# Kernel tuning notes

Hardware: AMD Instinct MI355X
Metric: run time of the kernel (lower is better)

## Reference

```python
import jax, jax.numpy as jnp
import numpy as np

B, IN_DIM, LATENT = 1024, 256, 256


def _linear_params(key, fan_in, fan_out):
    # torch nn.Linear default init: U(-1/sqrt(fan_in), 1/sqrt(fan_in))
    k1, k2 = jax.random.split(key)
    lim = 1.0 / np.sqrt(fan_in)
    W = jax.random.uniform(k1, (fan_out, fan_in), minval=-lim, maxval=lim, dtype=jnp.float32)
    b = jax.random.uniform(k2, (fan_out,), minval=-lim, maxval=lim, dtype=jnp.float32)
    return W, b


def setup_inputs() -> dict:
    key = jax.random.key(0)
    ks = jax.random.split(key, 8)
    Wd1, bd1 = _linear_params(ks[0], IN_DIM, LATENT)
    Wd2, bd2 = _linear_params(ks[1], LATENT, LATENT)
    Wu1, bu1 = _linear_params(ks[2], IN_DIM, LATENT)
    Wu2, bu2 = _linear_params(ks[3], LATENT, LATENT)
    Wm1, bm1 = _linear_params(ks[4], IN_DIM, LATENT)
    Wm2, bm2 = _linear_params(ks[5], LATENT, LATENT)
    x = jax.random.normal(ks[6], (B, IN_DIM), dtype=jnp.float32)
    v = jax.random.normal(ks[7], (B, LATENT), dtype=jnp.float32)  # noise from calculate_z
    return {
        "x": x,
        "Wd1": Wd1, "bd1": bd1, "Wd2": Wd2, "bd2": bd2,
        "Wu1": Wu1, "bu1": bu1, "Wu2": Wu2, "bu2": bu2,
        "Wm1": Wm1, "bm1": bm1, "Wm2": Wm2, "bm2": bm2,
        "v": v,
    }


def reference(x, Wd1, bd1, Wd2, bd2, Wu1, bu1, Wu2, bu2, Wm1, bm1, Wm2, bm2, v):
    sig = jax.nn.sigmoid
    # three small 2-layer MLPs
    d = sig(sig(x @ Wd1.T + bd1) @ Wd2.T + bd2)          # [B, n]
    u = sig(sig(x @ Wu1.T + bu1) @ Wu2.T + bu2)          # [B, n]
    mean = jnp.tanh(jnp.tanh(x @ Wm1.T + bm1) @ Wm2.T + bm2)  # [B, n]

    # calculate_r: inverse of diag_embed(d) is diag(1/d); +epsilon is added to ALL
    # entries (as in the original torch code), making D_inv a full matrix.
    EPS = 1e-6
    n = d.shape[-1]
    eye = jnp.eye(n, dtype=d.dtype)
    D_inv = (1.0 / d)[..., None] * eye + EPS               # [B, n, n]
    D_in_sqr = jnp.sqrt(D_inv)                             # elementwise sqrt
    U = u[:, :, None] * u[:, None, :]                      # rank-1 [B, n, n]
    ut_d_inv_u = jnp.einsum('bi,bij,bj->b', u, D_inv, u)[:, None, None]  # [B,1,1]
    eta = 1.0 / (1.0 + ut_d_inv_u)
    right = (1.0 - jnp.sqrt(eta)) / ut_d_inv_u
    R = D_in_sqr - right * jnp.matmul(D_inv, jnp.matmul(U, D_in_sqr))  # [B, n, n]

    # calculate_z
    z = jnp.einsum('bij,bj->bi', R, v) + mean              # [B, n]
    return (mean, R, z)
```

## Files before the change

kernel.cpp:

```cpp
#include <hip/hip_runtime.h>
#include <hip/hip_bf16.h>
#include <math.h>

#define NB 1024
#define N 256
#define NBN (NB * N)
#define EPS 1e-6f
#define SQRT_EPS 1e-3f

typedef short bf16x8 __attribute__((ext_vector_type(8)));
typedef float f32x4  __attribute__((ext_vector_type(4)));

__device__ __forceinline__ float fast_rcp(float x) {
    return __builtin_amdgcn_rcpf(x);
}
__device__ __forceinline__ float sigmoidf(float x) {
    return fast_rcp(1.0f + __expf(-x));
}
__device__ __forceinline__ float fast_tanh(float x) {
    float ax = fabsf(x);
    float e  = __expf(2.0f * ax);
    float t  = 1.0f - 2.0f * fast_rcp(e + 1.0f);
    return copysignf(t, x);
}
__device__ __forceinline__ unsigned short to_bf16(float f) {
    __hip_bfloat16 h = __float2bfloat16(f);
    return *(unsigned short*)&h;
}
__device__ __forceinline__ bf16x8 cvt8(float4 f0, float4 f1) {
    bf16x8 a;
    a[0] = (short)to_bf16(f0.x); a[1] = (short)to_bf16(f0.y);
    a[2] = (short)to_bf16(f0.z); a[3] = (short)to_bf16(f0.w);
    a[4] = (short)to_bf16(f1.x); a[5] = (short)to_bf16(f1.y);
    a[6] = (short)to_bf16(f1.z); a[7] = (short)to_bf16(f1.w);
    return a;
}

__global__ __launch_bounds__(768) void l1_kernel(
    const float* __restrict__ x,
    const float* __restrict__ Wd1, const float* __restrict__ Wu1,
    const float* __restrict__ Wm1,
    const float* __restrict__ bd1, const float* __restrict__ bu1,
    const float* __restrict__ bm1, unsigned short* __restrict__ h1g)
{
    const int tid = threadIdx.x;
    const int w   = tid >> 6;
    const int mlp = w >> 2;
    const int sub = w & 3;
    const int l   = tid & 63;
    const int ml  = l & 15;
    const int kg  = l >> 4;
    const int b0  = (blockIdx.x >> 2) * 16;
    const int n0  = (blockIdx.x & 3) * 64 + sub * 16;
    const int n   = n0 + ml;

    bf16x8 af[8];
    {
        const float* xrow = x + (size_t)(b0 + ml) * N;
        #pragma unroll
        for (int kq = 0; kq < 8; ++kq) {
            float4 f0 = *(const float4*)(xrow + kq * 32 + kg * 8);
            float4 f1 = *(const float4*)(xrow + kq * 32 + kg * 8 + 4);
            af[kq] = cvt8(f0, f1);
        }
    }
    const float* Wl = (mlp == 0) ? Wd1 : (mlp == 1) ? Wu1 : Wm1;
    const float* wrow = Wl + (size_t)n * N;
    f32x4 acc = {0.f, 0.f, 0.f, 0.f};
    #pragma unroll
    for (int kq = 0; kq < 8; ++kq) {
        float4 f0 = *(const float4*)(wrow + kq * 32 + kg * 8);
        float4 f1 = *(const float4*)(wrow + kq * 32 + kg * 8 + 4);
        bf16x8 bf = cvt8(f0, f1);
        acc = __builtin_amdgcn_mfma_f32_16x16x32_bf16(af[kq], bf, acc, 0, 0, 0);
    }
    const float* bias = (mlp == 0) ? bd1 : (mlp == 1) ? bu1 : bm1;
    const float bb = bias[n];
    #pragma unroll
    for (int reg = 0; reg < 4; ++reg) {
        const int row = b0 + kg * 4 + reg;
        float val = acc[reg] + bb;
        float act = (mlp < 2) ? sigmoidf(val) : fast_tanh(val);
        h1g[(size_t)mlp * NBN + (size_t)row * N + n] = to_bf16(act);
    }
}

__global__ __launch_bounds__(768) void l2_kernel(
    const unsigned short* __restrict__ h1g,
    const float* __restrict__ Wd2, const float* __restrict__ Wu2,
    const float* __restrict__ Wm2,
    const float* __restrict__ bd2, const float* __restrict__ bu2,
    const float* __restrict__ bm2, float* __restrict__ h2g)
{
    const int tid = threadIdx.x;
    const int w   = tid >> 6;
    const int mlp = w >> 2;
    const int sub = w & 3;
    const int l   = tid & 63;
    const int ml  = l & 15;
    const int kg  = l >> 4;
    const int b0  = (blockIdx.x >> 2) * 16;
    const int n0  = (blockIdx.x & 3) * 64 + sub * 16;
    const int n   = n0 + ml;

    bf16x8 af[8];
    {
        const unsigned short* arow = h1g + (size_t)mlp * NBN + (size_t)(b0 + ml) * N;
        #pragma unroll
        for (int kq = 0; kq < 8; ++kq)
            af[kq] = *(const bf16x8*)(arow + kq * 32 + kg * 8);
    }
    const float* Wl = (mlp == 0) ? Wd2 : (mlp == 1) ? Wu2 : Wm2;
    const float* wrow = Wl + (size_t)n * N;
    f32x4 acc = {0.f, 0.f, 0.f, 0.f};
    #pragma unroll
    for (int kq = 0; kq < 8; ++kq) {
        float4 f0 = *(const float4*)(wrow + kq * 32 + kg * 8);
        float4 f1 = *(const float4*)(wrow + kq * 32 + kg * 8 + 4);
        bf16x8 bf = cvt8(f0, f1);
        acc = __builtin_amdgcn_mfma_f32_16x16x32_bf16(af[kq], bf, acc, 0, 0, 0);
    }
    const float* bias = (mlp == 0) ? bd2 : (mlp == 1) ? bu2 : bm2;
    const float bb = bias[n];
    #pragma unroll
    for (int reg = 0; reg < 4; ++reg) {
        const int row = b0 + kg * 4 + reg;
        float val = acc[reg] + bb;
        float act = (mlp < 2) ? sigmoidf(val) : fast_tanh(val);
        h2g[(size_t)mlp * NBN + (size_t)row * N + n] = act;
    }
}

__global__ __launch_bounds__(256) void r_epi_kernel(
    const float* __restrict__ h2g, const float* __restrict__ v,
    float* __restrict__ out_mean, float* __restrict__ out_z,
    float* __restrict__ R)
{
    __shared__ float s_lds[N];
    __shared__ float a_lds[64];
    __shared__ float tp_lds[64];
    __shared__ float red1[4][3];
    __shared__ float red2[4];

    const int tid   = threadIdx.x;
    const int b     = blockIdx.x >> 2;
    const int chunk = blockIdx.x & 3;
    const int ibase = chunk * 64;
    const int lane  = tid & 63;
    const int wv    = tid >> 6;

    const float d_ = h2g[(size_t)0 * NBN + (size_t)b * N + tid];
    const float u_ = h2g[(size_t)1 * NBN + (size_t)b * N + tid];
    const float m_ = h2g[(size_t)2 * NBN + (size_t)b * N + tid];
    const float vv = v[(size_t)b * N + tid];
    const float inv_d = fast_rcp(d_);

    float s0 = u_, s1 = u_ * u_ * inv_d, s2 = vv;
    #pragma unroll
    for (int off = 32; off > 0; off >>= 1) {
        s0 += __shfl_down(s0, off, 64);
        s1 += __shfl_down(s1, off, 64);
        s2 += __shfl_down(s2, off, 64);
    }
    if (lane == 0) { red1[wv][0] = s0; red1[wv][1] = s1; red1[wv][2] = s2; }
    __syncthreads();
    const float Su = red1[0][0] + red1[1][0] + red1[2][0] + red1[3][0];
    const float qs = red1[0][1] + red1[1][1] + red1[2][1] + red1[3][1];
    const float Sv = red1[0][2] + red1[1][2] + red1[2][2] + red1[3][2];
    const float utDu  = qs + EPS * Su * Su;
    const float sqeta = rsqrtf(1.0f + utDu);
    const float right = (1.0f - sqeta) / utDu;
    const float a  = sqrtf(inv_d + EPS);
    const float s  = u_ * a + SQRT_EPS * (Su - u_);
    const float tp = right * (u_ * inv_d + EPS * Su);

    float sv = s * vv;
    #pragma unroll
    for (int off = 32; off > 0; off >>= 1)
        sv += __shfl_down(sv, off, 64);
    if (lane == 0) red2[wv] = sv;

    s_lds[tid] = s;
    if (tid >= ibase && tid < ibase + 64) {
        a_lds[tid - ibase]  = a;
        tp_lds[tid - ibase] = tp;
    }
    __syncthreads();
    sv = red2[0] + red2[1] + red2[2] + red2[3];

    if (chunk == 0) {
        const size_t idx = (size_t)b * N + tid;
        out_mean[idx] = m_;
        out_z[idx]    = SQRT_EPS * Sv + (a - SQRT_EPS) * vv - tp * sv + m_;
    }

    const int j4 = tid & 63;
    const int il = tid >> 6;
    const float4 svec = ((const float4*)s_lds)[j4];
    float4* Rb = (float4*)(R + (size_t)b * N * N);
    const int jb = j4 * 4;

    #pragma unroll
    for (int it = 0; it < 16; ++it) {
        const int i_loc = it * 4 + il;
        const int i     = ibase + i_loc;
        const float ai  = a_lds[i_loc];
        const float ti  = tp_lds[i_loc];
        float4 o;
        o.x = SQRT_EPS - ti * svec.x;
        o.y = SQRT_EPS - ti * svec.y;
        o.z = SQRT_EPS - ti * svec.z;
        o.w = SQRT_EPS - ti * svec.w;
        if (i >= jb && i < jb + 4) {
            const float add = ai - SQRT_EPS;
            if      (i == jb)     o.x += add;
            else if (i == jb + 1) o.y += add;
            else if (i == jb + 2) o.z += add;
            else                  o.w += add;
        }
        Rb[(size_t)i * 64 + j4] = o;
    }
}

extern "C" void kernel_launch(void* const* d_in, const int* in_sizes, int n_in,
                              void* d_out, int out_size, void* d_ws, size_t ws_size,
                              hipStream_t stream) {
    const float* x   = (const float*)d_in[0];
    const float* Wd1 = (const float*)d_in[1];
    const float* bd1 = (const float*)d_in[2];
    const float* Wd2 = (const float*)d_in[3];
    const float* bd2 = (const float*)d_in[4];
    const float* Wu1 = (const float*)d_in[5];
    const float* bu1 = (const float*)d_in[6];
    const float* Wu2 = (const float*)d_in[7];
    const float* bu2 = (const float*)d_in[8];
    const float* Wm1 = (const float*)d_in[9];
    const float* bm1 = (const float*)d_in[10];
    const float* Wm2 = (const float*)d_in[11];
    const float* bm2 = (const float*)d_in[12];
    const float* v   = (const float*)d_in[13];

    float* out      = (float*)d_out;
    float* out_mean = out;
    float* R        = out + (size_t)NB * N;
    float* out_z    = R + (size_t)NB * N * N;

    unsigned short* h1g = (unsigned short*)d_ws;
    float* h2g = (float*)(h1g + (size_t)3 * NBN);

    l1_kernel<<<256, 768, 0, stream>>>(x, Wd1, Wu1, Wm1, bd1, bu1, bm1, h1g);
    l2_kernel<<<256, 768, 0, stream>>>(h1g, Wd2, Wu2, Wm2, bd2, bu2, bm2, h2g);
    r_epi_kernel<<<NB * 4, 256, 0, stream>>>(h2g, v, out_mean, out_z, R);
}
```

Measured before the change: 72.16 us.

## Merge both MLP layers into one cooperative kernel with grid sync

The two separate layer kernels are combined into a single cooperative launch that uses a grid-wide barrier between layer 1 and layer 2, which removes one kernel launch and its gap. Input rows and layer-1 activations are now staged in shared memory once per block, so each wave reads the shared tile instead of reloading and reconverting global data. The cost is a cooperative-launch requirement and a grid sync. Launch fails if the 256 blocks of 768 threads cannot all be resident at once.

```diff
diff --git a/kernel.cpp b/kernel.cpp
--- a/kernel.cpp
+++ b/kernel.cpp
@@ -1,4 +1,5 @@
 #include <hip/hip_runtime.h>
+#include <hip/hip_cooperative_groups.h>
 #include <hip/hip_bf16.h>
 #include <math.h>
 
@@ -7,6 +8,8 @@
 #define NBN (NB * N)
 #define EPS 1e-6f
 #define SQRT_EPS 1e-3f
+
+namespace cg = cooperative_groups;
 
 typedef short bf16x8 __attribute__((ext_vector_type(8)));
 typedef float f32x4  __attribute__((ext_vector_type(4)));
@@ -36,13 +39,21 @@
     return a;
 }
 
-__global__ __launch_bounds__(768) void l1_kernel(
+__global__ __launch_bounds__(768) void coop_mlp_kernel(
     const float* __restrict__ x,
     const float* __restrict__ Wd1, const float* __restrict__ Wu1,
     const float* __restrict__ Wm1,
+    const float* __restrict__ Wd2, const float* __restrict__ Wu2,
+    const float* __restrict__ Wm2,
     const float* __restrict__ bd1, const float* __restrict__ bu1,
-    const float* __restrict__ bm1, unsigned short* __restrict__ h1g)
+    const float* __restrict__ bm1,
+    const float* __restrict__ bd2, const float* __restrict__ bu2,
+    const float* __restrict__ bm2,
+    unsigned short* __restrict__ h1g, float* __restrict__ h2g)
 {
+    __shared__ unsigned short xa[16][264];
+    __shared__ unsigned short hb[3][16][264];
+
     const int tid = threadIdx.x;
     const int w   = tid >> 6;
     const int mlp = w >> 2;
@@ -50,84 +61,82 @@
     const int l   = tid & 63;
     const int ml  = l & 15;
     const int kg  = l >> 4;
-    const int b0  = (blockIdx.x >> 2) * 16;
-    const int n0  = (blockIdx.x & 3) * 64 + sub * 16;
+    const int b0  = ((int)blockIdx.x >> 2) * 16;
+    const int n0  = ((int)blockIdx.x & 3) * 64 + sub * 16;
     const int n   = n0 + ml;
 
-    bf16x8 af[8];
+    if (tid < 512) {
+        const int row = tid >> 5;
+        const int c8  = tid & 31;
+        const float* src = x + (size_t)(b0 + row) * N + c8 * 8;
+        float4 f0 = *(const float4*)src;
+        float4 f1 = *(const float4*)(src + 4);
+        *(bf16x8*)&xa[row][c8 * 8] = cvt8(f0, f1);
+    }
+    __syncthreads();
+
     {
-        const float* xrow = x + (size_t)(b0 + ml) * N;
+        bf16x8 af[8];
+        #pragma unroll
+        for (int kq = 0; kq < 8; ++kq)
+            af[kq] = *(const bf16x8*)&xa[ml][kq * 32 + kg * 8];
+        const float* Wl = (mlp == 0) ? Wd1 : (mlp == 1) ? Wu1 : Wm1;
+        const float* wrow = Wl + (size_t)n * N;
+        f32x4 acc = {0.f, 0.f, 0.f, 0.f};
         #pragma unroll
         for (int kq = 0; kq < 8; ++kq) {
-            float4 f0 = *(const float4*)(xrow + kq * 32 + kg * 8);
-            float4 f1 = *(const float4*)(xrow + kq * 32 + kg * 8 + 4);
-            af[kq] = cvt8(f0, f1);
-        }
-    }
-    const float* Wl = (mlp == 0) ? Wd1 : (mlp == 1) ? Wu1 : Wm1;
-    const float* wrow = Wl + (size_t)n * N;
-    f32x4 acc = {0.f, 0.f, 0.f, 0.f};
-    #pragma unroll
-    for (int kq = 0; kq < 8; ++kq) {
-        float4 f0 = *(const float4*)(wrow + kq * 32 + kg * 8);
-        float4 f1 = *(const float4*)(wrow + kq * 32 + kg * 8 + 4);
-        bf16x8 bf = cvt8(f0, f1);
-        acc = __builtin_amdgcn_mfma_f32_16x16x32_bf16(af[kq], bf, acc, 0, 0, 0);
-    }
-    const float* bias = (mlp == 0) ? bd1 : (mlp == 1) ? bu1 : bm1;
-    const float bb = bias[n];
-    #pragma unroll
-    for (int reg = 0; reg < 4; ++reg) {
-        const int row = b0 + kg * 4 + reg;
-        float val = acc[reg] + bb;
-        float act = (mlp < 2) ? sigmoidf(val) : fast_tanh(val);
-        h1g[(size_t)mlp * NBN + (size_t)row * N + n] = to_bf16(act);
-    }
-}
-
-__global__ __launch_bounds__(768) void l2_kernel(
-    const unsigned short* __restrict__ h1g,
-    const float* __restrict__ Wd2, const float* __restrict__ Wu2,
-    const float* __restrict__ Wm2,
-    const float* __restrict__ bd2, const float* __restrict__ bu2,
-    const float* __restrict__ bm2, float* __restrict__ h2g)
-{
-    const int tid = threadIdx.x;
-    const int w   = tid >> 6;
-    const int mlp = w >> 2;
-    const int sub = w & 3;
-    const int l   = tid & 63;
-    const int ml  = l & 15;
-    const int kg  = l >> 4;
-    const int b0  = (blockIdx.x >> 2) * 16;
-    const int n0  = (blockIdx.x & 3) * 64 + sub * 16;
-    const int n   = n0 + ml;
-
-    bf16x8 af[8];
+            float4 f0 = *(const float4*)(wrow + kq * 32 + kg * 8);
+            float4 f1 = *(const float4*)(wrow + kq * 32 + kg * 8 + 4);
+            acc = __builtin_amdgcn_mfma_f32_16x16x32_bf16(af[kq], cvt8(f0, f1), acc, 0, 0, 0);
+        }
+        const float* bias = (mlp == 0) ? bd1 : (mlp == 1) ? bu1 : bm1;
+        const float bb = bias[n];
+        #pragma unroll
+        for (int reg = 0; reg < 4; ++reg) {
+            const int row = b0 + kg * 4 + reg;
+            float val = acc[reg] + bb;
+            float act = (mlp < 2) ? sigmoidf(val) : fast_tanh(val);
+            h1g[(size_t)mlp * NBN + (size_t)row * N + n] = to_bf16(act);
+        }
+    }
+
+    cg::this_grid().sync();
+
+    #pragma unroll
+    for (int t = 0; t < 2; ++t) {
+        const int idx = tid * 2 + t;
+        const int m2  = idx >> 9;
+        const int rem = idx & 511;
+        const int row = rem >> 5;
+        const int c8  = rem & 31;
+        *(bf16x8*)&hb[m2][row][c8 * 8] =
+            *(const bf16x8*)(h1g + (size_t)m2 * NBN + (size_t)(b0 + row) * N + c8 * 8);
+    }
+    __syncthreads();
+
     {
-        const unsigned short* arow = h1g + (size_t)mlp * NBN + (size_t)(b0 + ml) * N;
+        bf16x8 af[8];
         #pragma unroll
         for (int kq = 0; kq < 8; ++kq)
-            af[kq] = *(const bf16x8*)(arow + kq * 32 + kg * 8);
-    }
-    const float* Wl = (mlp == 0) ? Wd2 : (mlp == 1) ? Wu2 : Wm2;
-    const float* wrow = Wl + (size_t)n * N;
-    f32x4 acc = {0.f, 0.f, 0.f, 0.f};
-    #pragma unroll
-    for (int kq = 0; kq < 8; ++kq) {
-        float4 f0 = *(const float4*)(wrow + kq * 32 + kg * 8);
-        float4 f1 = *(const float4*)(wrow + kq * 32 + kg * 8 + 4);
-        bf16x8 bf = cvt8(f0, f1);
-        acc = __builtin_amdgcn_mfma_f32_16x16x32_bf16(af[kq], bf, acc, 0, 0, 0);
-    }
-    const float* bias = (mlp == 0) ? bd2 : (mlp == 1) ? bu2 : bm2;
-    const float bb = bias[n];
-    #pragma unroll
-    for (int reg = 0; reg < 4; ++reg) {
-        const int row = b0 + kg * 4 + reg;
-        float val = acc[reg] + bb;
-        float act = (mlp < 2) ? sigmoidf(val) : fast_tanh(val);
-        h2g[(size_t)mlp * NBN + (size_t)row * N + n] = act;
+            af[kq] = *(const bf16x8*)&hb[mlp][ml][kq * 32 + kg * 8];
+        const float* Wl = (mlp == 0) ? Wd2 : (mlp == 1) ? Wu2 : Wm2;
+        const float* wrow = Wl + (size_t)n * N;
+        f32x4 acc = {0.f, 0.f, 0.f, 0.f};
+        #pragma unroll
+        for (int kq = 0; kq < 8; ++kq) {
+            float4 f0 = *(const float4*)(wrow + kq * 32 + kg * 8);
+            float4 f1 = *(const float4*)(wrow + kq * 32 + kg * 8 + 4);
+            acc = __builtin_amdgcn_mfma_f32_16x16x32_bf16(af[kq], cvt8(f0, f1), acc, 0, 0, 0);
+        }
+        const float* bias = (mlp == 0) ? bd2 : (mlp == 1) ? bu2 : bm2;
+        const float bb = bias[n];
+        #pragma unroll
+        for (int reg = 0; reg < 4; ++reg) {
+            const int row = b0 + kg * 4 + reg;
+            float val = acc[reg] + bb;
+            float act = (mlp < 2) ? sigmoidf(val) : fast_tanh(val);
+            h2g[(size_t)mlp * NBN + (size_t)row * N + n] = act;
+        }
     }
 }
 
@@ -248,7 +257,16 @@
     unsigned short* h1g = (unsigned short*)d_ws;
     float* h2g = (float*)(h1g + (size_t)3 * NBN);
 
-    l1_kernel<<<256, 768, 0, stream>>>(x, Wd1, Wu1, Wm1, bd1, bu1, bm1, h1g);
-    l2_kernel<<<256, 768, 0, stream>>>(h1g, Wd2, Wu2, Wm2, bd2, bu2, bm2, h2g);
+    void* args[] = {
+        (void*)&x,
+        (void*)&Wd1, (void*)&Wu1, (void*)&Wm1,
+        (void*)&Wd2, (void*)&Wu2, (void*)&Wm2,
+        (void*)&bd1, (void*)&bu1, (void*)&bm1,
+        (void*)&bd2, (void*)&bu2, (void*)&bm2,
+        (void*)&h1g, (void*)&h2g
+    };
+    hipLaunchCooperativeKernel((const void*)coop_mlp_kernel,
+                               dim3(256), dim3(768), args, 0, stream);
+
     r_epi_kernel<<<NB * 4, 256, 0, stream>>>(h2g, v, out_mean, out_z, R);
 }
```

Result: slower. 100.1 us (+38.7%).
